# Optimization experiments

Hardware: AMD Instinct MI355X
Metric: run time of the kernel (lower is better)

The kernel has to match this reference:

```python
import jax, jax.numpy as jnp
import numpy as np

ALPHA = 10.0
BETA = 2.0
BASE = 0.5
N, D, N_CLASSES = 4096, 512, 128


def setup_inputs() -> dict:
    key = jax.random.key(0)
    k1, k2 = jax.random.split(key)
    x = jax.random.normal(k1, (N, D), dtype=jnp.float32)
    inputs = x / jnp.linalg.norm(x, axis=1, keepdims=True)  # L2-normalized embeddings
    targets = jax.random.randint(k2, (N,), 0, N_CLASSES, dtype=jnp.int64)
    margin = jnp.float32(0.5)
    return {"inputs": inputs, "targets": targets, "margin": margin}


def reference(inputs, targets, margin):
    # Vectorized equivalent of the per-row masked_select/sort/hard-mining loop.
    n = inputs.shape[0]
    sim = inputs @ inputs.T  # [n, n]
    same = targets[:, None] == targets[None, :]
    pos_mask = same & (sim < 1.0)        # positives, excluding self-sim == 1
    neg_mask = ~same

    # sort()[0] / sort()[-1]  ==  masked min / max
    min_pos = jnp.min(jnp.where(pos_mask, sim, jnp.inf), axis=1)    # pos_pair_[0]
    max_neg = jnp.max(jnp.where(neg_mask, sim, -jnp.inf), axis=1)   # neg_pair_[-1]

    # Hard mining: selected values equal the raw sims (the +/- margin and
    # min_pos/max_neg shifts cancel algebraically in the original code).
    sel_neg = neg_mask & (sim + margin - min_pos[:, None] > 0)
    sel_pos = pos_mask & (max_neg[:, None] - sim + margin > 0)

    pos_sum = jnp.sum(jnp.where(sel_pos, jnp.exp(-BETA * (sim - BASE)), 0.0), axis=1)
    neg_sum = jnp.sum(jnp.where(sel_neg, jnp.exp(ALPHA * (sim - BASE)), 0.0), axis=1)
    row_loss = (2.0 / BETA) * jnp.log1p(pos_sum) + (2.0 / ALPHA) * jnp.log1p(neg_sum)

    # Rows with no surviving pos or neg pairs are skipped (counted in c).
    valid = jnp.any(sel_pos, axis=1) & jnp.any(sel_neg, axis=1)
    loss = jnp.sum(jnp.where(valid, row_loss, 0.0)) / n
    prec = jnp.mean((~valid).astype(jnp.float32))

    # Original returns mean sims of the LAST row's (pre-mining) pos/neg pairs.
    lp = pos_mask[-1].astype(sim.dtype)
    ln = neg_mask[-1].astype(sim.dtype)
    mean_pos_sim = jnp.sum(sim[-1] * lp) / jnp.maximum(jnp.sum(lp), 1.0)
    mean_neg_sim = jnp.sum(sim[-1] * ln) / jnp.maximum(jnp.sum(ln), 1.0)
    return (loss, prec, mean_pos_sim, mean_neg_sim)
```

## Files before the change

### kernel.cpp

```cpp
#include <hip/hip_runtime.h>
#include <hip/hip_bf16.h>
#include <math.h>

#define NROWS 4096
#define DDIM  512
#define BM    128
#define BK    32
#define NT    (DDIM / BK)
#define NBLK  (NROWS / BM)
#define NTRI  (NBLK * (NBLK + 1) / 2)

static constexpr float ALPHA = 10.0f;
static constexpr float BETA  = 2.0f;
static constexpr float BASE  = 0.5f;

typedef short bf16x8 __attribute__((ext_vector_type(8)));
typedef float f32x4 __attribute__((ext_vector_type(4)));

__device__ __forceinline__ unsigned f2bf(float f) {
  __hip_bfloat16 h = __float2bfloat16(f);
  return (unsigned)*reinterpret_cast<unsigned short*>(&h);
}
__device__ __forceinline__ float bf2f(unsigned short u) {
  return __uint_as_float(((unsigned)u) << 16);
}

#define GLOAD_LDS16(g, l)                                              \
  __builtin_amdgcn_global_load_lds(                                    \
      (const __attribute__((address_space(1))) void*)(g),              \
      (__attribute__((address_space(3))) void*)(l), 16, 0, 0)

__global__ __launch_bounds__(256) void convert_k(const float* __restrict__ X,
                                                 unsigned short* __restrict__ Xb) {
  const int wid = threadIdx.x >> 6, lane = threadIdx.x & 63;
  const int r = blockIdx.x * 4 + wid;
  const size_t base = (size_t)r * DDIM + lane * 8;
  const float4 v0 = *reinterpret_cast<const float4*>(X + base);
  const float4 v1 = *reinterpret_cast<const float4*>(X + base + 4);
  uint4 u;
  u.x = f2bf(v0.x) | (f2bf(v0.y) << 16);
  u.y = f2bf(v0.z) | (f2bf(v0.w) << 16);
  u.z = f2bf(v1.x) | (f2bf(v1.y) << 16);
  u.w = f2bf(v1.z) | (f2bf(v1.w) << 16);
  *reinterpret_cast<uint4*>(Xb + base) = u;
}

__global__ __launch_bounds__(256) void gemm_tri_store(
    const unsigned short* __restrict__ Xb, unsigned short* __restrict__ simb) {
  __shared__ unsigned short SH[2][BM * BK] __attribute__((aligned(16)));

  int kk0 = blockIdx.x, bi = 0;
  while (kk0 >= NBLK - bi) { kk0 -= NBLK - bi; ++bi; }
  const int bj = bi + kk0;
  const int i0 = bi * BM, j0 = bj * BM;
  const bool diagb = (bi == bj);

  const int tid = threadIdx.x;
  const int w = tid >> 6, lane = tid & 63;
  const int wr = w >> 1, wc = w & 1;
  const int g = lane >> 4, q = lane & 15;
  const char* Xbb = (const char*)Xb;

  f32x4 acc[4][4];
  #pragma unroll
  for (int m = 0; m < 4; ++m)
    #pragma unroll
    for (int n = 0; n < 4; ++n) acc[m][n] = (f32x4)0.0f;

  for (int t = 0; t < NT; ++t) {
    #pragma unroll
    for (int l = 0; l < 2; ++l) {
      const int lin = (l * 256 + tid) * 16;
      const int row = lin >> 6;
      const int col = lin & 63;
      GLOAD_LDS16(Xbb + (size_t)(i0 + row) * (DDIM * 2) + t * (BK * 2) + col,
                  (char*)&SH[0][0] + lin);
      if (!diagb)
        GLOAD_LDS16(Xbb + (size_t)(j0 + row) * (DDIM * 2) + t * (BK * 2) + col,
                    (char*)&SH[1][0] + lin);
    }
    __syncthreads();
    const char* Ab = (const char*)&SH[0][0];
    const char* Bb = diagb ? Ab : (const char*)&SH[1][0];
    bf16x8 a[4], b[4];
    #pragma unroll
    for (int fm = 0; fm < 4; ++fm)
      a[fm] = *reinterpret_cast<const bf16x8*>(Ab + (wr * 64 + fm * 16 + q) * 64 + g * 16);
    #pragma unroll
    for (int fn = 0; fn < 4; ++fn)
      b[fn] = *reinterpret_cast<const bf16x8*>(Bb + (wc * 64 + fn * 16 + q) * 64 + g * 16);
    #pragma unroll
    for (int fm = 0; fm < 4; ++fm)
      #pragma unroll
      for (int fn = 0; fn < 4; ++fn)
        acc[fm][fn] = __builtin_amdgcn_mfma_f32_16x16x32_bf16(a[fm], b[fn], acc[fm][fn], 0, 0, 0);
    __syncthreads();
  }

  unsigned short* SV = &SH[0][0];
  #pragma unroll
  for (int orient = 0; orient < 2; ++orient) {
    if (orient == 1 && diagb) break;
    for (int d = 0; d < 4; ++d) {
      if (orient == 0) {
        if (wr == (d >> 1)) {
          #pragma unroll
          for (int h = 0; h < 2; ++h) {
            const int fm = 2 * (d & 1) + h;
            #pragma unroll
            for (int fn = 0; fn < 4; ++fn)
              #pragma unroll
              for (int reg = 0; reg < 4; ++reg) {
                const int shrow = h * 16 + g * 4 + reg;
                const int col = wc * 64 + fn * 16 + q;
                unsigned short v = (unsigned short)f2bf(acc[fm][fn][reg]);
                if (diagb && (32 * d + shrow == col)) v = 0x3F80;
                SV[shrow * 136 + col] = v;
              }
          }
        }
      } else {
        if (wc == (d >> 1)) {
          #pragma unroll
          for (int h = 0; h < 2; ++h) {
            const int fn = 2 * (d & 1) + h;
            const int shrow = h * 16 + q;
            #pragma unroll
            for (int fm = 0; fm < 4; ++fm) {
              const int colR = wr * 64 + fm * 16 + g * 4;
              uint2 uu;
              uu.x = f2bf(acc[fm][fn][0]) | (f2bf(acc[fm][fn][1]) << 16);
              uu.y = f2bf(acc[fm][fn][2]) | (f2bf(acc[fm][fn][3]) << 16);
              *reinterpret_cast<uint2*>(&SV[shrow * 136 + colR]) = uu;
            }
          }
        }
      }
      __syncthreads();
      #pragma unroll
      for (int rr = 0; rr < 2; ++rr) {
        const int s = tid + rr * 256;
        const int row = s >> 4, cs = s & 15;
        const bf16x8 vv = *reinterpret_cast<const bf16x8*>(&SV[row * 136 + cs * 8]);
        unsigned short* dst =
            (orient == 0)
                ? simb + (size_t)(i0 + d * 32 + row) * NROWS + j0 + cs * 8
                : simb + (size_t)(j0 + d * 32 + row) * NROWS + i0 + cs * 8;
        *reinterpret_cast<bf16x8*>(dst) = vv;
      }
      __syncthreads();
    }
  }
}

__global__ __launch_bounds__(256) void rows_k(
    const unsigned short* __restrict__ simb, const int* __restrict__ tgt,
    const float* __restrict__ marginp, float* __restrict__ rowloss,
    float* __restrict__ rowvalid, float* __restrict__ lacc) {
  __shared__ int tgl[NROWS];
  const int tid = threadIdx.x;
  #pragma unroll
  for (int c = 0; c < 4; ++c)
    reinterpret_cast<int4*>(tgl)[tid + c * 256] =
        reinterpret_cast<const int4*>(tgt)[tid + c * 256];
  __syncthreads();

  const int wid = tid >> 6, lane = tid & 63;
  const int i = blockIdx.x * 4 + wid;
  const int ti = tgl[i];
  const unsigned short* row = simb + (size_t)i * NROWS;
  const bool lastw = (i == NROWS - 1);

  bf16x8 v[8];
  unsigned long long same = 0ull;
  float minp = INFINITY, maxn = -INFINITY;
  #pragma unroll
  for (int c = 0; c < 8; ++c) {
    const int j0 = c * 512 + lane * 8;
    v[c] = *reinterpret_cast<const bf16x8*>(row + j0);
    const int4 t0 = *reinterpret_cast<const int4*>(tgl + j0);
    const int4 t1 = *reinterpret_cast<const int4*>(tgl + j0 + 4);
    const int tj[8] = {t0.x, t0.y, t0.z, t0.w, t1.x, t1.y, t1.z, t1.w};
    #pragma unroll
    for (int e = 0; e < 8; ++e) {
      const float s = bf2f((unsigned short)v[c][e]);
      const bool sm = (tj[e] == ti);
      same |= (unsigned long long)sm << (c * 8 + e);
      if (sm) {
        if (s < 1.0f) minp = fminf(minp, s);
      } else {
        maxn = fmaxf(maxn, s);
      }
    }
  }
  #pragma unroll
  for (int off = 1; off < 64; off <<= 1) {
    minp = fminf(minp, __shfl_xor(minp, off));
    maxn = fmaxf(maxn, __shfl_xor(maxn, off));
  }

  const float margin = *marginp;
  float psum = 0.0f, nsum = 0.0f;
  float lsp = 0.0f, lcp = 0.0f, lsn = 0.0f, lcn = 0.0f;
  #pragma unroll
  for (int c = 0; c < 8; ++c) {
    #pragma unroll
    for (int e = 0; e < 8; ++e) {
      const float s = bf2f((unsigned short)v[c][e]);
      const bool sm = (same >> (c * 8 + e)) & 1ull;
      if (!sm) {
        if (s + margin - minp > 0.0f) nsum += __expf(ALPHA * (s - BASE));
        if (lastw) { lsn += s; lcn += 1.0f; }
      } else if (s < 1.0f) {
        if (maxn - s + margin > 0.0f) psum += __expf(-BETA * (s - BASE));
        if (lastw) { lsp += s; lcp += 1.0f; }
      }
    }
  }
  #pragma unroll
  for (int off = 1; off < 64; off <<= 1) {
    psum += __shfl_xor(psum, off);
    nsum += __shfl_xor(nsum, off);
  }
  if (lastw) {
    #pragma unroll
    for (int off = 1; off < 64; off <<= 1) {
      lsp += __shfl_xor(lsp, off); lcp += __shfl_xor(lcp, off);
      lsn += __shfl_xor(lsn, off); lcn += __shfl_xor(lcn, off);
    }
  }
  if (lane == 0) {
    const bool valid = (psum > 0.0f) && (nsum > 0.0f);
    rowloss[i] = valid ? (2.0f / BETA) * log1pf(psum) + (2.0f / ALPHA) * log1pf(nsum) : 0.0f;
    rowvalid[i] = valid ? 0.0f : 1.0f;
    if (lastw) { lacc[0] = lsp; lacc[1] = lcp; lacc[2] = lsn; lacc[3] = lcn; }
  }
}

__device__ __forceinline__ float block_sum(float v) {
  __shared__ float sh[4];
  #pragma unroll
  for (int off = 32; off > 0; off >>= 1) v += __shfl_down(v, off);
  if ((threadIdx.x & 63) == 0) sh[threadIdx.x >> 6] = v;
  __syncthreads();
  float r = sh[0] + sh[1] + sh[2] + sh[3];
  __syncthreads();
  return r;
}

__global__ __launch_bounds__(256) void finalize_k(
    const float* __restrict__ rowloss, const float* __restrict__ rowvalid,
    const float* __restrict__ lacc, float* __restrict__ out) {
  float lsum = 0.0f, inval = 0.0f;
  #pragma unroll
  for (int c = 0; c < 16; ++c) {
    const int i = c * 256 + threadIdx.x;
    lsum += rowloss[i];
    inval += rowvalid[i];
  }
  lsum = block_sum(lsum);
  inval = block_sum(inval);
  if (threadIdx.x == 0) {
    out[0] = lsum / (float)NROWS;
    out[1] = inval / (float)NROWS;
    out[2] = lacc[0] / fmaxf(lacc[1], 1.0f);
    out[3] = lacc[2] / fmaxf(lacc[3], 1.0f);
  }
}

extern "C" void kernel_launch(void* const* d_in, const int* in_sizes, int n_in,
                              void* d_out, int out_size, void* d_ws, size_t ws_size,
                              hipStream_t stream) {
  const float* X = (const float*)d_in[0];
  const int* tgt = (const int*)d_in[1];
  const float* marginp = (const float*)d_in[2];
  float* out = (float*)d_out;

  char* ws = (char*)d_ws;
  float* rowloss = (float*)ws;
  float* rowvalid = (float*)(ws + (16 << 10));
  float* lacc = (float*)(ws + (32 << 10));
  unsigned short* Xb = (unsigned short*)(ws + (128 << 10));
  unsigned short* simb = (unsigned short*)(ws + (128 << 10) + ((size_t)4 << 20));

  convert_k<<<dim3(NROWS / 4), 256, 0, stream>>>(X, Xb);
  gemm_tri_store<<<dim3(NTRI), 256, 0, stream>>>(Xb, simb);
  rows_k<<<dim3(NROWS / 4), 256, 0, stream>>>(simb, tgt, marginp, rowloss, rowvalid, lacc);
  finalize_k<<<dim3(1), 256, 0, stream>>>(rowloss, rowvalid, lacc, out);
}
```

Baseline: 116.0 us.

## Fuse row min/max mining into GEMM epilogue with atomics and double-buffer LDS

Computes per-row positive-min and negative-max in the GEMM epilogue from fp32 accumulators, covering both the tile and its mirrored transpose, and merges them through order-preserving encoded atomicMin/atomicMax into global buffers initialized by the convert kernel. The rows kernel then reads these values and makes a single pass over each sim row instead of two, so it no longer needs to keep the row in registers. The GEMM main loop also gains LDS double buffering so the next k-tile loads while the current one computes, and block indices are swizzled. Costs are extra epilogue work, shuffles and global atomics. Min/max are now taken on fp32 rather than bf16-rounded values, which may shift borderline mining decisions slightly.

```diff
diff --git a/kernel.cpp b/kernel.cpp
--- a/kernel.cpp
+++ b/kernel.cpp
@@ -17,6 +17,14 @@
 typedef short bf16x8 __attribute__((ext_vector_type(8)));
 typedef float f32x4 __attribute__((ext_vector_type(4)));
 
+__device__ __forceinline__ unsigned enc_f32(float f) {
+  unsigned b = __float_as_uint(f);
+  return (b & 0x80000000u) ? ~b : (b | 0x80000000u);
+}
+__device__ __forceinline__ float dec_f32(unsigned u) {
+  unsigned b = (u & 0x80000000u) ? (u & 0x7fffffffu) : ~u;
+  return __uint_as_float(b);
+}
 __device__ __forceinline__ unsigned f2bf(float f) {
   __hip_bfloat16 h = __float2bfloat16(f);
   return (unsigned)*reinterpret_cast<unsigned short*>(&h);
@@ -31,7 +39,14 @@
       (__attribute__((address_space(3))) void*)(l), 16, 0, 0)
 
 __global__ __launch_bounds__(256) void convert_k(const float* __restrict__ X,
-                                                 unsigned short* __restrict__ Xb) {
+                                                 unsigned short* __restrict__ Xb,
+                                                 unsigned* __restrict__ minb,
+                                                 unsigned* __restrict__ maxb) {
+  const int gid = blockIdx.x * 256 + threadIdx.x;
+  if (gid < NROWS) {
+    minb[gid] = 0xFF800000u;
+    maxb[gid] = 0x007FFFFFu;
+  }
   const int wid = threadIdx.x >> 6, lane = threadIdx.x & 63;
   const int r = blockIdx.x * 4 + wid;
   const size_t base = (size_t)r * DDIM + lane * 8;
@@ -46,10 +61,13 @@
 }
 
 __global__ __launch_bounds__(256) void gemm_tri_store(
-    const unsigned short* __restrict__ Xb, unsigned short* __restrict__ simb) {
-  __shared__ unsigned short SH[2][BM * BK] __attribute__((aligned(16)));
-
-  int kk0 = blockIdx.x, bi = 0;
+    const unsigned short* __restrict__ Xb, const int* __restrict__ tgt,
+    unsigned* __restrict__ minb, unsigned* __restrict__ maxb,
+    unsigned short* __restrict__ simb) {
+  __shared__ unsigned short lds[2][2][BM * BK] __attribute__((aligned(16)));
+
+  const int bswz = (blockIdx.x & 7) * (NTRI / 8) + (blockIdx.x >> 3);
+  int kk0 = bswz, bi = 0;
   while (kk0 >= NBLK - bi) { kk0 -= NBLK - bi; ++bi; }
   const int bj = bi + kk0;
   const int i0 = bi * BM, j0 = bj * BM;
@@ -67,21 +85,29 @@
     #pragma unroll
     for (int n = 0; n < 4; ++n) acc[m][n] = (f32x4)0.0f;
 
+  #define STAGE(buf, t)                                                        \
+    do {                                                                       \
+      const int kb_ = (t) * (BK * 2);                                          \
+      _Pragma("unroll")                                                        \
+      for (int l_ = 0; l_ < 2; ++l_) {                                         \
+        const int lin_ = (l_ * 256 + tid) * 16;                                \
+        const int row_ = lin_ >> 6;                                            \
+        const int col_ = lin_ & 63;                                            \
+        GLOAD_LDS16(Xbb + (size_t)(i0 + row_) * (DDIM * 2) + kb_ + col_,       \
+                    (char*)&lds[buf][0][0] + lin_);                            \
+        if (!diagb)                                                            \
+          GLOAD_LDS16(Xbb + (size_t)(j0 + row_) * (DDIM * 2) + kb_ + col_,     \
+                      (char*)&lds[buf][1][0] + lin_);                          \
+      }                                                                        \
+    } while (0)
+
+  STAGE(0, 0);
+  __syncthreads();
+  int cur = 0;
   for (int t = 0; t < NT; ++t) {
-    #pragma unroll
-    for (int l = 0; l < 2; ++l) {
-      const int lin = (l * 256 + tid) * 16;
-      const int row = lin >> 6;
-      const int col = lin & 63;
-      GLOAD_LDS16(Xbb + (size_t)(i0 + row) * (DDIM * 2) + t * (BK * 2) + col,
-                  (char*)&SH[0][0] + lin);
-      if (!diagb)
-        GLOAD_LDS16(Xbb + (size_t)(j0 + row) * (DDIM * 2) + t * (BK * 2) + col,
-                    (char*)&SH[1][0] + lin);
-    }
-    __syncthreads();
-    const char* Ab = (const char*)&SH[0][0];
-    const char* Bb = diagb ? Ab : (const char*)&SH[1][0];
+    if (t + 1 < NT) STAGE(cur ^ 1, t + 1);
+    const char* Ab = (const char*)&lds[cur][0][0];
+    const char* Bb = diagb ? Ab : (const char*)&lds[cur][1][0];
     bf16x8 a[4], b[4];
     #pragma unroll
     for (int fm = 0; fm < 4; ++fm)
@@ -95,9 +121,82 @@
       for (int fn = 0; fn < 4; ++fn)
         acc[fm][fn] = __builtin_amdgcn_mfma_f32_16x16x32_bf16(a[fm], b[fn], acc[fm][fn], 0, 0, 0);
     __syncthreads();
-  }
-
-  unsigned short* SV = &SH[0][0];
+    cur ^= 1;
+  }
+
+  const int rbase = i0 + wr * 64;
+  int cg[4], tj[4], cloc[4];
+  #pragma unroll
+  for (int fn = 0; fn < 4; ++fn) {
+    cloc[fn] = wc * 64 + fn * 16 + q;
+    cg[fn] = j0 + cloc[fn];
+    tj[fn] = tgt[cg[fn]];
+  }
+  int ti16[16];
+  #pragma unroll
+  for (int fm = 0; fm < 4; ++fm)
+    #pragma unroll
+    for (int reg = 0; reg < 4; ++reg)
+      ti16[fm * 4 + reg] = tgt[rbase + fm * 16 + g * 4 + reg];
+
+  #pragma unroll
+  for (int fm = 0; fm < 4; ++fm) {
+    #pragma unroll
+    for (int reg = 0; reg < 4; ++reg) {
+      const int rloc = wr * 64 + fm * 16 + g * 4 + reg;
+      const int r = i0 + rloc;
+      const int tr = ti16[fm * 4 + reg];
+      float mnp = INFINITY, mxn = -INFINITY;
+      #pragma unroll
+      for (int fn = 0; fn < 4; ++fn) {
+        float s = acc[fm][fn][reg];
+        if (diagb && rloc == cloc[fn]) s = 1.0f;
+        if (tj[fn] == tr) {
+          if (s < 1.0f) mnp = fminf(mnp, s);
+        } else {
+          mxn = fmaxf(mxn, s);
+        }
+      }
+      #pragma unroll
+      for (int off = 1; off < 16; off <<= 1) {
+        mnp = fminf(mnp, __shfl_xor(mnp, off));
+        mxn = fmaxf(mxn, __shfl_xor(mxn, off));
+      }
+      if (q == 0) {
+        if (mnp != INFINITY) atomicMin(minb + r, enc_f32(mnp));
+        if (mxn != -INFINITY) atomicMax(maxb + r, enc_f32(mxn));
+      }
+    }
+  }
+  if (!diagb) {
+    #pragma unroll
+    for (int fn = 0; fn < 4; ++fn) {
+      const int tc = tj[fn];
+      float mnp = INFINITY, mxn = -INFINITY;
+      #pragma unroll
+      for (int fm = 0; fm < 4; ++fm)
+        #pragma unroll
+        for (int reg = 0; reg < 4; ++reg) {
+          const float s = acc[fm][fn][reg];
+          if (ti16[fm * 4 + reg] == tc) {
+            if (s < 1.0f) mnp = fminf(mnp, s);
+          } else {
+            mxn = fmaxf(mxn, s);
+          }
+        }
+      mnp = fminf(mnp, __shfl_xor(mnp, 16));
+      mnp = fminf(mnp, __shfl_xor(mnp, 32));
+      mxn = fmaxf(mxn, __shfl_xor(mxn, 16));
+      mxn = fmaxf(mxn, __shfl_xor(mxn, 32));
+      if (lane < 16) {
+        if (mnp != INFINITY) atomicMin(minb + cg[fn], enc_f32(mnp));
+        if (mxn != -INFINITY) atomicMax(maxb + cg[fn], enc_f32(mxn));
+      }
+    }
+  }
+
+  unsigned short* SV = &lds[0][0][0];
+  __syncthreads();
   #pragma unroll
   for (int orient = 0; orient < 2; ++orient) {
     if (orient == 1 && diagb) break;
@@ -155,6 +254,7 @@
 
 __global__ __launch_bounds__(256) void rows_k(
     const unsigned short* __restrict__ simb, const int* __restrict__ tgt,
+    const unsigned* __restrict__ minb, const unsigned* __restrict__ maxb,
     const float* __restrict__ marginp, float* __restrict__ rowloss,
     float* __restrict__ rowvalid, float* __restrict__ lacc) {
   __shared__ int tgl[NROWS];
@@ -168,47 +268,25 @@
   const int wid = tid >> 6, lane = tid & 63;
   const int i = blockIdx.x * 4 + wid;
   const int ti = tgl[i];
+  const float minp = dec_f32(minb[i]);
+  const float maxn = dec_f32(maxb[i]);
+  const float margin = *marginp;
   const unsigned short* row = simb + (size_t)i * NROWS;
   const bool lastw = (i == NROWS - 1);
 
-  bf16x8 v[8];
-  unsigned long long same = 0ull;
-  float minp = INFINITY, maxn = -INFINITY;
+  float psum = 0.0f, nsum = 0.0f;
+  float lsp = 0.0f, lcp = 0.0f, lsn = 0.0f, lcn = 0.0f;
   #pragma unroll
   for (int c = 0; c < 8; ++c) {
     const int j0 = c * 512 + lane * 8;
-    v[c] = *reinterpret_cast<const bf16x8*>(row + j0);
+    const bf16x8 v = *reinterpret_cast<const bf16x8*>(row + j0);
     const int4 t0 = *reinterpret_cast<const int4*>(tgl + j0);
     const int4 t1 = *reinterpret_cast<const int4*>(tgl + j0 + 4);
     const int tj[8] = {t0.x, t0.y, t0.z, t0.w, t1.x, t1.y, t1.z, t1.w};
     #pragma unroll
     for (int e = 0; e < 8; ++e) {
-      const float s = bf2f((unsigned short)v[c][e]);
-      const bool sm = (tj[e] == ti);
-      same |= (unsigned long long)sm << (c * 8 + e);
-      if (sm) {
-        if (s < 1.0f) minp = fminf(minp, s);
-      } else {
-        maxn = fmaxf(maxn, s);
-      }
-    }
-  }
-  #pragma unroll
-  for (int off = 1; off < 64; off <<= 1) {
-    minp = fminf(minp, __shfl_xor(minp, off));
-    maxn = fmaxf(maxn, __shfl_xor(maxn, off));
-  }
-
-  const float margin = *marginp;
-  float psum = 0.0f, nsum = 0.0f;
-  float lsp = 0.0f, lcp = 0.0f, lsn = 0.0f, lcn = 0.0f;
-  #pragma unroll
-  for (int c = 0; c < 8; ++c) {
-    #pragma unroll
-    for (int e = 0; e < 8; ++e) {
-      const float s = bf2f((unsigned short)v[c][e]);
-      const bool sm = (same >> (c * 8 + e)) & 1ull;
-      if (!sm) {
+      const float s = bf2f((unsigned short)v[e]);
+      if (tj[e] != ti) {
         if (s + margin - minp > 0.0f) nsum += __expf(ALPHA * (s - BASE));
         if (lastw) { lsn += s; lcn += 1.0f; }
       } else if (s < 1.0f) {
@@ -280,11 +358,14 @@
   float* rowloss = (float*)ws;
   float* rowvalid = (float*)(ws + (16 << 10));
   float* lacc = (float*)(ws + (32 << 10));
+  unsigned* minb = (unsigned*)(ws + (48 << 10));
+  unsigned* maxb = (unsigned*)(ws + (64 << 10));
   unsigned short* Xb = (unsigned short*)(ws + (128 << 10));
   unsigned short* simb = (unsigned short*)(ws + (128 << 10) + ((size_t)4 << 20));
 
-  convert_k<<<dim3(NROWS / 4), 256, 0, stream>>>(X, Xb);
-  gemm_tri_store<<<dim3(NTRI), 256, 0, stream>>>(Xb, simb);
-  rows_k<<<dim3(NROWS / 4), 256, 0, stream>>>(simb, tgt, marginp, rowloss, rowvalid, lacc);
+  convert_k<<<dim3(NROWS / 4), 256, 0, stream>>>(X, Xb, minb, maxb);
+  gemm_tri_store<<<dim3(NTRI), 256, 0, stream>>>(Xb, tgt, minb, maxb, simb);
+  rows_k<<<dim3(NROWS / 4), 256, 0, stream>>>(simb, tgt, minb, maxb, marginp,
+                                              rowloss, rowvalid, lacc);
   finalize_k<<<dim3(1), 256, 0, stream>>>(rowloss, rowvalid, lacc, out);
 }
```

Measured after the change: 127.6 us. +10.0%, slower.

## Widen K tile to 128 with XOR-swizzled LDS and block-index swizzle

Applied to the files above, without the earlier changes.

Raises the K tile from 32 to 128, so each block does four MFMA k-steps per barrier pair instead of one. This cuts the number of global-to-LDS load phases and __syncthreads per tile. The global source columns are XOR-swizzled on load and the same swizzle is applied on LDS reads to avoid bank conflicts from the wider 256-byte row stride. Block indices are also permuted across the triangular tile set to spread work and L2 access. LDS use grows to 64KB per block, which may lower occupancy.

```diff
diff --git a/kernel.cpp b/kernel.cpp
--- a/kernel.cpp
+++ b/kernel.cpp
@@ -5,7 +5,7 @@
 #define NROWS 4096
 #define DDIM  512
 #define BM    128
-#define BK    32
+#define BK    128
 #define NT    (DDIM / BK)
 #define NBLK  (NROWS / BM)
 #define NTRI  (NBLK * (NBLK + 1) / 2)
@@ -47,9 +47,10 @@
 
 __global__ __launch_bounds__(256) void gemm_tri_store(
     const unsigned short* __restrict__ Xb, unsigned short* __restrict__ simb) {
-  __shared__ unsigned short SH[2][BM * BK] __attribute__((aligned(16)));
-
-  int kk0 = blockIdx.x, bi = 0;
+  __shared__ unsigned short lds[2][BM * BK] __attribute__((aligned(16)));
+
+  const int bswz = (blockIdx.x & 7) * (NTRI / 8) + (blockIdx.x >> 3);
+  int kk0 = bswz, bi = 0;
   while (kk0 >= NBLK - bi) { kk0 -= NBLK - bi; ++bi; }
   const int bj = bi + kk0;
   const int i0 = bi * BM, j0 = bj * BM;
@@ -68,36 +69,49 @@
     for (int n = 0; n < 4; ++n) acc[m][n] = (f32x4)0.0f;
 
   for (int t = 0; t < NT; ++t) {
-    #pragma unroll
-    for (int l = 0; l < 2; ++l) {
-      const int lin = (l * 256 + tid) * 16;
-      const int row = lin >> 6;
-      const int col = lin & 63;
-      GLOAD_LDS16(Xbb + (size_t)(i0 + row) * (DDIM * 2) + t * (BK * 2) + col,
-                  (char*)&SH[0][0] + lin);
-      if (!diagb)
-        GLOAD_LDS16(Xbb + (size_t)(j0 + row) * (DDIM * 2) + t * (BK * 2) + col,
-                    (char*)&SH[1][0] + lin);
+    {
+      const int kb = t * (BK * 2);
+      #pragma unroll
+      for (int c = 0; c < 8; ++c) {
+        const int lin = (c * 256 + tid) * 16;
+        const int row = lin >> 8;
+        const int col = lin & 255;
+        const int scol = col ^ ((row & 15) << 4);
+        GLOAD_LDS16(Xbb + (size_t)(i0 + row) * (DDIM * 2) + kb + scol,
+                    (char*)&lds[0][0] + lin);
+        if (!diagb)
+          GLOAD_LDS16(Xbb + (size_t)(j0 + row) * (DDIM * 2) + kb + scol,
+                      (char*)&lds[1][0] + lin);
+      }
     }
     __syncthreads();
-    const char* Ab = (const char*)&SH[0][0];
-    const char* Bb = diagb ? Ab : (const char*)&SH[1][0];
-    bf16x8 a[4], b[4];
-    #pragma unroll
-    for (int fm = 0; fm < 4; ++fm)
-      a[fm] = *reinterpret_cast<const bf16x8*>(Ab + (wr * 64 + fm * 16 + q) * 64 + g * 16);
-    #pragma unroll
-    for (int fn = 0; fn < 4; ++fn)
-      b[fn] = *reinterpret_cast<const bf16x8*>(Bb + (wc * 64 + fn * 16 + q) * 64 + g * 16);
-    #pragma unroll
-    for (int fm = 0; fm < 4; ++fm)
-      #pragma unroll
-      for (int fn = 0; fn < 4; ++fn)
-        acc[fm][fn] = __builtin_amdgcn_mfma_f32_16x16x32_bf16(a[fm], b[fn], acc[fm][fn], 0, 0, 0);
+    const char* Ab = (const char*)&lds[0][0];
+    const char* Bb = diagb ? Ab : (const char*)&lds[1][0];
+    #pragma unroll
+    for (int kk = 0; kk < 4; ++kk) {
+      bf16x8 a[4], b[4];
+      #pragma unroll
+      for (int fm = 0; fm < 4; ++fm) {
+        const int row = wr * 64 + fm * 16 + q;
+        const int colb = (kk * 64 + g * 16) ^ ((row & 15) << 4);
+        a[fm] = *reinterpret_cast<const bf16x8*>(Ab + row * 256 + colb);
+      }
+      #pragma unroll
+      for (int fn = 0; fn < 4; ++fn) {
+        const int row = wc * 64 + fn * 16 + q;
+        const int colb = (kk * 64 + g * 16) ^ ((row & 15) << 4);
+        b[fn] = *reinterpret_cast<const bf16x8*>(Bb + row * 256 + colb);
+      }
+      #pragma unroll
+      for (int fm = 0; fm < 4; ++fm)
+        #pragma unroll
+        for (int fn = 0; fn < 4; ++fn)
+          acc[fm][fn] = __builtin_amdgcn_mfma_f32_16x16x32_bf16(a[fm], b[fn], acc[fm][fn], 0, 0, 0);
+    }
     __syncthreads();
   }
 
-  unsigned short* SV = &SH[0][0];
+  unsigned short* SV = &lds[0][0];
   #pragma unroll
   for (int orient = 0; orient < 2; ++orient) {
     if (orient == 1 && diagb) break;
```

After: 110.2 us. 5.0% less time.
